# Performance work log

Hardware: AMD Instinct MI355X
Metric: run time of the kernel (lower is better)

The kernel has to match this reference:

```python
import jax, jax.numpy as jnp
from jax import lax
import numpy as np

B, S, N, F, H = 8, 64, 256, 16, 16
C = N * H  # temporal conv channels = 4096
ALPHA = 0.2
EPS = 1e-5
NEG = -9e15


def setup_inputs() -> dict:
    key = jax.random.key(0)
    ks = jax.random.split(key, 10)
    x = jax.random.normal(ks[0], (B, S, N, F), dtype=jnp.float32)
    adj = jax.random.normal(ks[1], (N, N), dtype=jnp.float32)
    W = jax.random.normal(ks[2], (F, H), dtype=jnp.float32) * (1.414 / np.sqrt(F))
    a = jax.random.normal(ks[3], (2 * H,), dtype=jnp.float32) * (1.414 / np.sqrt(2 * H))
    a1, a2 = a[:H], a[H:]
    conv_w = jax.random.normal(ks[4], (C, C, 3), dtype=jnp.float32) * (1.0 / np.sqrt(C * 3))
    conv_b = jnp.zeros((C,), dtype=jnp.float32)
    bn_gamma = jnp.ones((C,), dtype=jnp.float32)
    bn_beta = jnp.zeros((C,), dtype=jnp.float32)
    bn_mean = jnp.zeros((C,), dtype=jnp.float32)
    bn_var = jnp.ones((C,), dtype=jnp.float32)
    ln_gamma = jnp.ones((H,), dtype=jnp.float32)
    ln_beta = jnp.zeros((H,), dtype=jnp.float32)
    return {"x": x, "adj": adj, "W": W, "a1": a1, "a2": a2,
            "conv_w": conv_w, "conv_b": conv_b,
            "bn_gamma": bn_gamma, "bn_beta": bn_beta,
            "bn_mean": bn_mean, "bn_var": bn_var,
            "ln_gamma": ln_gamma, "ln_beta": ln_beta}


def reference(x, adj, W, a1, a2, conv_w, conv_b, bn_gamma, bn_beta, bn_mean, bn_var, ln_gamma, ln_beta):
    b, s, n, f = x.shape
    h = W.shape[1]
    # --- GAT, batched over all timesteps (eval mode: dropout is identity) ---
    Wh = jnp.einsum('bsnf,fh->bsnh', x, W)            # (B,S,N,H)
    # e_ij = LeakyReLU(a1.Wh_i + a2.Wh_j), equivalent to concat-then-matmul
    f1 = jnp.einsum('bsnh,h->bsn', Wh, a1)
    f2 = jnp.einsum('bsnh,h->bsn', Wh, a2)
    e = jax.nn.leaky_relu(f1[..., :, None] + f2[..., None, :], ALPHA)  # (B,S,N,N)
    e = jnp.where(adj > 0, e, NEG)
    attn = jax.nn.softmax(e, axis=-1)
    spatial = jnp.einsum('bsij,bsjh->bsih', attn, Wh)  # (B,S,N,H)
    # --- temporal conv over seq dim, channels = N*H ---
    t = spatial.reshape(b, s, n * h).transpose(0, 2, 1)  # (B,C,S)
    y = lax.conv_general_dilated(t, conv_w, window_strides=(1,), padding=[(1, 1)],
                                 dimension_numbers=('NCH', 'OIH', 'NCH'))
    y = y + conv_b[None, :, None]
    # BatchNorm1d in eval mode
    y = (y - bn_mean[None, :, None]) / jnp.sqrt(bn_var + EPS)[None, :, None]
    y = y * bn_gamma[None, :, None] + bn_beta[None, :, None]
    y = jax.nn.relu(y)
    temp = y.transpose(0, 2, 1).reshape(b, s, n, h)
    # residual is identity since in_features == hidden_dim
    out = temp + x
    # LayerNorm over last dim
    mu = out.mean(-1, keepdims=True)
    var = out.var(-1, keepdims=True)
    out = (out - mu) / jnp.sqrt(var + EPS) * ln_gamma + ln_beta
    return out
```

## Files before the change

kernel.cpp:

```cpp
#include <hip/hip_runtime.h>
#include <stdint.h>

#define ALPHA 0.2f
#define EPSV  1e-5f

typedef unsigned short u16;
typedef unsigned int   u32;
typedef unsigned long long u64;
typedef __bf16 bf16x8 __attribute__((ext_vector_type(8)));
typedef float  f32x4  __attribute__((ext_vector_type(4)));

#define NB 8
#define NS 64
#define NN 256
#define NF 16
#define NH 16
#define NC 4096
#define NK 12288
#define NP 512

__device__ __forceinline__ u16 f2b(float f){
  u32 u = __float_as_uint(f);
  u32 r = u + 0x7fffu + ((u>>16)&1u);
  return (u16)(r>>16);
}
__device__ __forceinline__ u32 pack2(float a, float b){ return (u32)f2b(a) | ((u32)f2b(b)<<16); }
__device__ __forceinline__ void gld16(void* lds, const void* g){
  __builtin_amdgcn_global_load_lds((const __attribute__((address_space(1))) u32*)g,
                                   (__attribute__((address_space(3))) u32*)lds, 16, 0, 0);
}

__global__ __launch_bounds__(256) void k_adj(const float* __restrict__ adj,
                                             u64* __restrict__ am){
  int w = threadIdx.x>>6, l = threadIdx.x&63;
  int row = blockIdx.x*4 + w;
  #pragma unroll
  for(int g=0;g<4;g++){
    float v = adj[(size_t)row*NN + g*64 + l];
    u64 m = __ballot(v > 0.f);
    if(l==0) am[row*4+g] = m;
  }
}

__global__ __launch_bounds__(256) void k_cw(const float* __restrict__ cw,
                                            u16* __restrict__ bw){
  size_t i = ((size_t)blockIdx.x*256 + threadIdx.x)*8;
  f32x4 f0 = ((const f32x4*)(cw+i))[0];
  f32x4 f1v = ((const f32x4*)(cw+i))[1];
  uint4 o;
  o.x = pack2(f0[0],f0[1]); o.y = pack2(f0[2],f0[3]);
  o.z = pack2(f1v[0],f1v[1]); o.w = pack2(f1v[2],f1v[3]);
  *(uint4*)(bw+i) = o;
}

__global__ __launch_bounds__(256) void k_attn(
    const float* __restrict__ x, const float* __restrict__ W,
    const float* __restrict__ a1, const float* __restrict__ a2,
    const u64* __restrict__ am, u16* __restrict__ Bt){
  __shared__ __align__(16) float Ws[NF][NH];
  __shared__ float a1s[NH], a2s[NH];
  __shared__ __align__(16) float Whs[NN][NH];
  __shared__ float f2s[NN];
  int t = threadIdx.x, bs = blockIdx.x;
  int b = bs>>6, s = bs&63;
  Ws[t>>4][t&15] = W[t];
  if(t<NH){ a1s[t]=a1[t]; a2s[t]=a2[t]; }
  u64 mg[4];
  #pragma unroll
  for(int g=0;g<4;g++) mg[g] = am[t*4+g];
  __syncthreads();

  const float* xp = x + ((size_t)bs*NN + t)*NF;
  float xr[16];
  #pragma unroll
  for(int g=0;g<4;g++) *(f32x4*)&xr[g*4] = ((const f32x4*)xp)[g];
  float wh[16];
  #pragma unroll
  for(int h=0;h<16;h++) wh[h]=0.f;
  #pragma unroll
  for(int f=0;f<16;f++){
    float xf = xr[f];
    #pragma unroll
    for(int h=0;h<16;h++) wh[h] = fmaf(xf, Ws[f][h], wh[h]);
  }
  float fi=0.f, s2=0.f;
  #pragma unroll
  for(int h=0;h<16;h++){ fi=fmaf(wh[h],a1s[h],fi); s2=fmaf(wh[h],a2s[h],s2); }
  #pragma unroll
  for(int g=0;g<4;g++) ((f32x4*)Whs[t])[g] = *(f32x4*)&wh[g*4];
  f2s[t] = s2;
  __syncthreads();

  float den = 0.f;
  f32x4 a0={0,0,0,0}, a1v={0,0,0,0}, a2v={0,0,0,0}, a3v={0,0,0,0};
  #pragma unroll
  for(int g=0;g<4;g++){
    u64 mm = mg[g];
    for(int jj=0;jj<64;jj++){
      int j = g*64+jj;
      float e = fi + f2s[j];
      e = e > 0.f ? e : ALPHA*e;
      float p = ((mm>>jj)&1ull) ? __expf(e) : 0.f;
      den += p;
      const f32x4* wr = (const f32x4*)Whs[j];
      a0 += wr[0]*p; a1v += wr[1]*p; a2v += wr[2]*p; a3v += wr[3]*p;
    }
  }
  float inv = 1.f/fmaxf(den, 1e-30f);
  float vals[16];
  *(f32x4*)&vals[0]  = a0*inv;  *(f32x4*)&vals[4]  = a1v*inv;
  *(f32x4*)&vals[8]  = a2v*inv; *(f32x4*)&vals[12] = a3v*inv;

  #pragma unroll
  for(int k=0;k<3;k++){
    int cs = s + 1 - k;
    if(cs >= 0 && cs < NS){
      size_t base = ((size_t)(b*NS+cs))*NK + (size_t)t*48 + k;
      #pragma unroll
      for(int h=0;h<16;h++) Bt[base + h*3] = f2b(vals[h]);
    }
  }
  if(s == 0){
    size_t base = ((size_t)(b*NS))*NK + (size_t)t*48;
    #pragma unroll
    for(int h=0;h<16;h++) Bt[base + h*3] = 0;
  }
  if(s == NS-1){
    size_t base = ((size_t)(b*NS+NS-1))*NK + (size_t)t*48 + 2;
    #pragma unroll
    for(int h=0;h<16;h++) Bt[base + h*3] = 0;
  }
}

__global__ __launch_bounds__(256) void k_gemm(
    const u16* __restrict__ Abt, const u16* __restrict__ Bw,
    float* __restrict__ yp, int kchunk){
  __shared__ __align__(16) u16 As0[128*32];
  __shared__ __align__(16) u16 As1[128*32];
  __shared__ __align__(16) u16 Bs0[128*32];
  __shared__ __align__(16) u16 Bs1[128*32];
  int t = threadIdx.x;
  int id = blockIdx.x;
  int xr_ = id & 7, q0 = id >> 3;
  int mI = q0 & 3, nhi = q0 >> 2;
  int m0 = mI*128, n0 = (nhi*8 + xr_)*128;
  int kbeg = blockIdx.y*kchunk;
  f32x4 acc[4][4];
  #pragma unroll
  for(int i=0;i<4;i++)
    #pragma unroll
    for(int j=0;j<4;j++) acc[i][j] = (f32x4){0,0,0,0};

  int l = t&63, w = t>>6;
  int wm = (w&1)*64, wn = (w>>1)*64;
  int q = l>>4, r16 = l&15;

  int c0 = t, c1 = t+256;
  const u16* ga0 = Abt + (size_t)(m0 + (c0>>2))*NK + (c0&3)*8;
  const u16* ga1 = Abt + (size_t)(m0 + (c1>>2))*NK + (c1&3)*8;
  const u16* gb0 = Bw  + (size_t)(n0 + (c0>>2))*NK + (c0&3)*8;
  const u16* gb1 = Bw  + (size_t)(n0 + (c1>>2))*NK + (c1&3)*8;
  u16 *la00 = As0 + c0*8, *la01 = As0 + c1*8;
  u16 *la10 = As1 + c0*8, *la11 = As1 + c1*8;
  u16 *lb00 = Bs0 + c0*8, *lb01 = Bs0 + c1*8;
  u16 *lb10 = Bs1 + c0*8, *lb11 = Bs1 + c1*8;

  for(int kk=0; kk<kchunk; kk+=64){
    int k0 = kbeg + kk;
    __syncthreads();
    gld16(la00, ga0 + k0);      gld16(la01, ga1 + k0);
    gld16(lb00, gb0 + k0);      gld16(lb01, gb1 + k0);
    gld16(la10, ga0 + k0 + 32); gld16(la11, ga1 + k0 + 32);
    gld16(lb10, gb0 + k0 + 32); gld16(lb11, gb1 + k0 + 32);
    __syncthreads();
    {
      bf16x8 af[4], bfr[4];
      #pragma unroll
      for(int mt=0;mt<4;mt++) af[mt]  = *(const bf16x8*)(As0 + (wm+mt*16+r16)*32 + q*8);
      #pragma unroll
      for(int nt=0;nt<4;nt++) bfr[nt] = *(const bf16x8*)(Bs0 + (wn+nt*16+r16)*32 + q*8);
      #pragma unroll
      for(int mt=0;mt<4;mt++)
        #pragma unroll
        for(int nt=0;nt<4;nt++)
          acc[mt][nt] = __builtin_amdgcn_mfma_f32_16x16x32_bf16(af[mt], bfr[nt], acc[mt][nt], 0,0,0);
    }
    {
      bf16x8 af[4], bfr[4];
      #pragma unroll
      for(int mt=0;mt<4;mt++) af[mt]  = *(const bf16x8*)(As1 + (wm+mt*16+r16)*32 + q*8);
      #pragma unroll
      for(int nt=0;nt<4;nt++) bfr[nt] = *(const bf16x8*)(Bs1 + (wn+nt*16+r16)*32 + q*8);
      #pragma unroll
      for(int mt=0;mt<4;mt++)
        #pragma unroll
        for(int nt=0;nt<4;nt++)
          acc[mt][nt] = __builtin_amdgcn_mfma_f32_16x16x32_bf16(af[mt], bfr[nt], acc[mt][nt], 0,0,0);
    }
  }
  float* op = yp + (size_t)blockIdx.y*NP*NC;
  #pragma unroll
  for(int mt=0;mt<4;mt++)
    #pragma unroll
    for(int nt=0;nt<4;nt++)
      #pragma unroll
      for(int rr=0;rr<4;rr++){
        int m = m0 + wm + mt*16 + q*4 + rr;
        int n = n0 + wn + nt*16 + r16;
        op[(size_t)m*NC + n] = acc[mt][nt][rr];
      }
}

__global__ __launch_bounds__(256) void k_post(
    const float* __restrict__ yp, int nparts,
    const float* __restrict__ x,
    const float* __restrict__ cb, const float* __restrict__ bg,
    const float* __restrict__ bb, const float* __restrict__ bm,
    const float* __restrict__ bv, const float* __restrict__ lg,
    const float* __restrict__ lb, float* __restrict__ out){
  int n = threadIdx.x, bs = blockIdx.x;
  float v[16];
  #pragma unroll
  for(int g=0;g<4;g++){
    f32x4 sum = {0,0,0,0};
    for(int p=0;p<nparts;p++)
      sum += ((const f32x4*)(yp + (size_t)p*NP*NC + (size_t)bs*NC + n*16))[g];
    *(f32x4*)&v[g*4] = sum;
  }
  const float* xp = x + ((size_t)bs*NN + n)*NH;
  float xr[16];
  #pragma unroll
  for(int g=0;g<4;g++) *(f32x4*)&xr[g*4] = ((const f32x4*)xp)[g];

  float mu = 0.f;
  #pragma unroll
  for(int h=0;h<16;h++){
    int co = n*16 + h;
    float t1 = v[h] + cb[co];
    t1 = (t1 - bm[co]) * (1.f/sqrtf(bv[co] + EPSV));
    t1 = t1 * bg[co] + bb[co];
    t1 = fmaxf(t1, 0.f);
    t1 += xr[h];
    v[h] = t1; mu += t1;
  }
  mu *= (1.f/16.f);
  float var = 0.f;
  #pragma unroll
  for(int h=0;h<16;h++){ float d = v[h]-mu; var = fmaf(d,d,var); }
  var *= (1.f/16.f);
  float rs = 1.f/sqrtf(var + EPSV);
  float* op = out + ((size_t)bs*NN + n)*NH;
  #pragma unroll
  for(int h=0;h<16;h++) op[h] = (v[h]-mu)*rs*lg[h] + lb[h];
}

extern "C" void kernel_launch(void* const* d_in, const int* in_sizes, int n_in,
                              void* d_out, int out_size, void* d_ws, size_t ws_size,
                              hipStream_t stream){
  const float* x   = (const float*)d_in[0];
  const float* adj = (const float*)d_in[1];
  const float* W   = (const float*)d_in[2];
  const float* a1  = (const float*)d_in[3];
  const float* a2  = (const float*)d_in[4];
  const float* cw  = (const float*)d_in[5];
  const float* cb  = (const float*)d_in[6];
  const float* bg  = (const float*)d_in[7];
  const float* bb  = (const float*)d_in[8];
  const float* bm  = (const float*)d_in[9];
  const float* bv  = (const float*)d_in[10];
  const float* lg  = (const float*)d_in[11];
  const float* lb  = (const float*)d_in[12];
  float* out = (float*)d_out;

  char* ws = (char*)d_ws;
  const size_t AM_OFF = 0;
  const size_t BT_OFF = AM_OFF + (size_t)NN*4*8;
  const size_t BW_OFF = BT_OFF + (size_t)NP*NK*2;
  const size_t YP_OFF = BW_OFF + (size_t)NC*NK*2;
  const size_t ypb    = (size_t)NP*NC*4;
  int P = 1;
  if(ws_size >= YP_OFF + 8*ypb)      P = 8;
  else if(ws_size >= YP_OFF + 4*ypb) P = 4;
  else if(ws_size >= YP_OFF + 2*ypb) P = 2;

  u64*   am  = (u64*)  (ws + AM_OFF);
  u16*   Bt  = (u16*)  (ws + BT_OFF);
  u16*   Bw  = (u16*)  (ws + BW_OFF);
  float* yp  = (float*)(ws + YP_OFF);

  hipLaunchKernelGGL(k_adj,  dim3(64),        dim3(256), 0, stream, adj, am);
  hipLaunchKernelGGL(k_cw,   dim3(NC*NK/(256*8)), dim3(256), 0, stream, cw, Bw);
  hipLaunchKernelGGL(k_attn, dim3(NP),        dim3(256), 0, stream, x,W,a1,a2,am,Bt);
  hipLaunchKernelGGL(k_gemm, dim3(128,P),     dim3(256), 0, stream, Bt, Bw, yp, NK/P);
  hipLaunchKernelGGL(k_post, dim3(NP),        dim3(256), 0, stream, yp,P,x,cb,bg,bb,bm,bv,lg,lb,out);
}
```

Baseline: 501.2 us.

## Fuse conv-weight bf16 conversion into GEMM loads and store bf16 partial sums

Drops the separate kernel that converts the 4096x12288 fp32 conv weights to bf16. The GEMM now reads fp32 weights directly, converts them in registers and writes them to LDS, so the bf16 copy is never written to or reread from memory. Partial GEMM outputs are also stored as bf16 rather than fp32, halving split-K workspace traffic, which costs accuracy in the summed results. The B-operand path becomes synchronous register loads instead of async global-to-LDS loads, and each 128-row weight tile is now fetched as fp32 by every block that uses it, with no prefetch overlap.

```diff
diff --git a/kernel.cpp b/kernel.cpp
--- a/kernel.cpp
+++ b/kernel.cpp
@@ -8,6 +8,7 @@
 typedef unsigned int   u32;
 typedef unsigned long long u64;
 typedef __bf16 bf16x8 __attribute__((ext_vector_type(8)));
+typedef __bf16 bf16x2 __attribute__((ext_vector_type(2)));
 typedef float  f32x4  __attribute__((ext_vector_type(4)));
 
 #define NB 8
@@ -25,9 +26,20 @@
   return (u16)(r>>16);
 }
 __device__ __forceinline__ u32 pack2(float a, float b){ return (u32)f2b(a) | ((u32)f2b(b)<<16); }
+__device__ __forceinline__ void un2(u32 v, float& lo, float& hi){
+  lo = __uint_as_float(v<<16); hi = __uint_as_float(v & 0xffff0000u);
+}
 __device__ __forceinline__ void gld16(void* lds, const void* g){
   __builtin_amdgcn_global_load_lds((const __attribute__((address_space(1))) u32*)g,
                                    (__attribute__((address_space(3))) u32*)lds, 16, 0, 0);
+}
+__device__ __forceinline__ uint4 cvt8(f32x4 a, f32x4 b){
+  union { uint4 u; bf16x2 h[4]; } r;
+  r.h[0] = (bf16x2){(__bf16)a[0], (__bf16)a[1]};
+  r.h[1] = (bf16x2){(__bf16)a[2], (__bf16)a[3]};
+  r.h[2] = (bf16x2){(__bf16)b[0], (__bf16)b[1]};
+  r.h[3] = (bf16x2){(__bf16)b[2], (__bf16)b[3]};
+  return r.u;
 }
 
 __global__ __launch_bounds__(256) void k_adj(const float* __restrict__ adj,
@@ -40,17 +52,6 @@
     u64 m = __ballot(v > 0.f);
     if(l==0) am[row*4+g] = m;
   }
-}
-
-__global__ __launch_bounds__(256) void k_cw(const float* __restrict__ cw,
-                                            u16* __restrict__ bw){
-  size_t i = ((size_t)blockIdx.x*256 + threadIdx.x)*8;
-  f32x4 f0 = ((const f32x4*)(cw+i))[0];
-  f32x4 f1v = ((const f32x4*)(cw+i))[1];
-  uint4 o;
-  o.x = pack2(f0[0],f0[1]); o.y = pack2(f0[2],f0[3]);
-  o.z = pack2(f1v[0],f1v[1]); o.w = pack2(f1v[2],f1v[3]);
-  *(uint4*)(bw+i) = o;
 }
 
 __global__ __launch_bounds__(256) void k_attn(
@@ -133,8 +134,8 @@
 }
 
 __global__ __launch_bounds__(256) void k_gemm(
-    const u16* __restrict__ Abt, const u16* __restrict__ Bw,
-    float* __restrict__ yp, int kchunk){
+    const u16* __restrict__ Abt, const float* __restrict__ Bwf,
+    u16* __restrict__ yp, int kchunk){
   __shared__ __align__(16) u16 As0[128*32];
   __shared__ __align__(16) u16 As1[128*32];
   __shared__ __align__(16) u16 Bs0[128*32];
@@ -156,10 +157,10 @@
   int q = l>>4, r16 = l&15;
 
   int c0 = t, c1 = t+256;
-  const u16* ga0 = Abt + (size_t)(m0 + (c0>>2))*NK + (c0&3)*8;
-  const u16* ga1 = Abt + (size_t)(m0 + (c1>>2))*NK + (c1&3)*8;
-  const u16* gb0 = Bw  + (size_t)(n0 + (c0>>2))*NK + (c0&3)*8;
-  const u16* gb1 = Bw  + (size_t)(n0 + (c1>>2))*NK + (c1&3)*8;
+  const u16*   ga0 = Abt + (size_t)(m0 + (c0>>2))*NK + (c0&3)*8;
+  const u16*   ga1 = Abt + (size_t)(m0 + (c1>>2))*NK + (c1&3)*8;
+  const float* gb0 = Bwf + (size_t)(n0 + (c0>>2))*NK + (c0&3)*8;
+  const float* gb1 = Bwf + (size_t)(n0 + (c1>>2))*NK + (c1&3)*8;
   u16 *la00 = As0 + c0*8, *la01 = As0 + c1*8;
   u16 *la10 = As1 + c0*8, *la11 = As1 + c1*8;
   u16 *lb00 = Bs0 + c0*8, *lb01 = Bs0 + c1*8;
@@ -167,11 +168,23 @@
 
   for(int kk=0; kk<kchunk; kk+=64){
     int k0 = kbeg + kk;
+    f32x4 v00a = *(const f32x4*)(gb0 + k0);
+    f32x4 v00b = *(const f32x4*)(gb0 + k0 + 4);
+    f32x4 v01a = *(const f32x4*)(gb1 + k0);
+    f32x4 v01b = *(const f32x4*)(gb1 + k0 + 4);
+    f32x4 v10a = *(const f32x4*)(gb0 + k0 + 32);
+    f32x4 v10b = *(const f32x4*)(gb0 + k0 + 36);
+    f32x4 v11a = *(const f32x4*)(gb1 + k0 + 32);
+    f32x4 v11b = *(const f32x4*)(gb1 + k0 + 36);
+    uint4 w00 = cvt8(v00a, v00b);
+    uint4 w01 = cvt8(v01a, v01b);
+    uint4 w10 = cvt8(v10a, v10b);
+    uint4 w11 = cvt8(v11a, v11b);
     __syncthreads();
     gld16(la00, ga0 + k0);      gld16(la01, ga1 + k0);
-    gld16(lb00, gb0 + k0);      gld16(lb01, gb1 + k0);
     gld16(la10, ga0 + k0 + 32); gld16(la11, ga1 + k0 + 32);
-    gld16(lb10, gb0 + k0 + 32); gld16(lb11, gb1 + k0 + 32);
+    *(uint4*)lb00 = w00; *(uint4*)lb01 = w01;
+    *(uint4*)lb10 = w10; *(uint4*)lb11 = w11;
     __syncthreads();
     {
       bf16x8 af[4], bfr[4];
@@ -198,7 +211,7 @@
           acc[mt][nt] = __builtin_amdgcn_mfma_f32_16x16x32_bf16(af[mt], bfr[nt], acc[mt][nt], 0,0,0);
     }
   }
-  float* op = yp + (size_t)blockIdx.y*NP*NC;
+  u16* op = yp + (size_t)blockIdx.y*NP*NC;
   #pragma unroll
   for(int mt=0;mt<4;mt++)
     #pragma unroll
@@ -207,12 +220,12 @@
       for(int rr=0;rr<4;rr++){
         int m = m0 + wm + mt*16 + q*4 + rr;
         int n = n0 + wn + nt*16 + r16;
-        op[(size_t)m*NC + n] = acc[mt][nt][rr];
+        op[(size_t)m*NC + n] = f2b(acc[mt][nt][rr]);
       }
 }
 
 __global__ __launch_bounds__(256) void k_post(
-    const float* __restrict__ yp, int nparts,
+    const u16* __restrict__ yp, int nparts,
     const float* __restrict__ x,
     const float* __restrict__ cb, const float* __restrict__ bg,
     const float* __restrict__ bb, const float* __restrict__ bm,
@@ -221,11 +234,20 @@
   int n = threadIdx.x, bs = blockIdx.x;
   float v[16];
   #pragma unroll
-  for(int g=0;g<4;g++){
-    f32x4 sum = {0,0,0,0};
-    for(int p=0;p<nparts;p++)
-      sum += ((const f32x4*)(yp + (size_t)p*NP*NC + (size_t)bs*NC + n*16))[g];
-    *(f32x4*)&v[g*4] = sum;
+  for(int h=0;h<16;h++) v[h]=0.f;
+  for(int p=0;p<nparts;p++){
+    const u16* pp = yp + (size_t)p*NP*NC + (size_t)bs*NC + n*16;
+    uint4 u0 = ((const uint4*)pp)[0];
+    uint4 u1 = ((const uint4*)pp)[1];
+    float lo, hi;
+    un2(u0.x,lo,hi); v[0]+=lo;  v[1]+=hi;
+    un2(u0.y,lo,hi); v[2]+=lo;  v[3]+=hi;
+    un2(u0.z,lo,hi); v[4]+=lo;  v[5]+=hi;
+    un2(u0.w,lo,hi); v[6]+=lo;  v[7]+=hi;
+    un2(u1.x,lo,hi); v[8]+=lo;  v[9]+=hi;
+    un2(u1.y,lo,hi); v[10]+=lo; v[11]+=hi;
+    un2(u1.z,lo,hi); v[12]+=lo; v[13]+=hi;
+    un2(u1.w,lo,hi); v[14]+=lo; v[15]+=hi;
   }
   const float* xp = x + ((size_t)bs*NN + n)*NH;
   float xr[16];
@@ -275,9 +297,8 @@
   char* ws = (char*)d_ws;
   const size_t AM_OFF = 0;
   const size_t BT_OFF = AM_OFF + (size_t)NN*4*8;
-  const size_t BW_OFF = BT_OFF + (size_t)NP*NK*2;
-  const size_t YP_OFF = BW_OFF + (size_t)NC*NK*2;
-  const size_t ypb    = (size_t)NP*NC*4;
+  const size_t YP_OFF = BT_OFF + (size_t)NP*NK*2;
+  const size_t ypb    = (size_t)NP*NC*2;
   int P = 1;
   if(ws_size >= YP_OFF + 8*ypb)      P = 8;
   else if(ws_size >= YP_OFF + 4*ypb) P = 4;
@@ -285,12 +306,10 @@
 
   u64*   am  = (u64*)  (ws + AM_OFF);
   u16*   Bt  = (u16*)  (ws + BT_OFF);
-  u16*   Bw  = (u16*)  (ws + BW_OFF);
-  float* yp  = (float*)(ws + YP_OFF);
-
-  hipLaunchKernelGGL(k_adj,  dim3(64),        dim3(256), 0, stream, adj, am);
-  hipLaunchKernelGGL(k_cw,   dim3(NC*NK/(256*8)), dim3(256), 0, stream, cw, Bw);
-  hipLaunchKernelGGL(k_attn, dim3(NP),        dim3(256), 0, stream, x,W,a1,a2,am,Bt);
-  hipLaunchKernelGGL(k_gemm, dim3(128,P),     dim3(256), 0, stream, Bt, Bw, yp, NK/P);
-  hipLaunchKernelGGL(k_post, dim3(NP),        dim3(256), 0, stream, yp,P,x,cb,bg,bb,bm,bv,lg,lb,out);
-}
+  u16*   yp  = (u16*)  (ws + YP_OFF);
+
+  hipLaunchKernelGGL(k_adj,  dim3(64),    dim3(256), 0, stream, adj, am);
+  hipLaunchKernelGGL(k_attn, dim3(NP),    dim3(256), 0, stream, x,W,a1,a2,am,Bt);
+  hipLaunchKernelGGL(k_gemm, dim3(128,P), dim3(256), 0, stream, Bt, cw, yp, NK/P);
+  hipLaunchKernelGGL(k_post, dim3(NP),    dim3(256), 0, stream, yp,P,x,cb,bg,bb,bm,bv,lg,lb,out);
+}
```

New measurement: 426.7 us. -14.9%, faster.
